# Kernel tuning notes

Hardware: AMD Instinct MI355X
Metric: run time of the kernel (lower is better)

The kernel has to match this reference:

```python
import jax, jax.numpy as jnp
import numpy as np

NUM_EXPERTS = 7
TRUNK_DIM = 64
HIDDEN = 64   # max(48, trunk_dim)
NUM_DEPTH_CLASSES = 3
BATCH = 262144


def setup_inputs() -> dict:
    key = jax.random.key(0)
    ks = jax.random.split(key, 8)
    trunk_feat = jax.random.normal(ks[0], (BATCH, TRUNK_DIM), dtype=jnp.float32)
    size_idx = jax.random.randint(ks[1], (BATCH,), 0, NUM_EXPERTS, dtype=jnp.int64)
    # Stacked expert MLP params: Linear(64,64) -> ReLU -> Linear(64,64) -> ReLU -> Linear(64,3)
    s1 = 1.0 / np.sqrt(TRUNK_DIM)
    s2 = 1.0 / np.sqrt(HIDDEN)
    W1 = jax.random.uniform(ks[2], (NUM_EXPERTS, TRUNK_DIM, HIDDEN), jnp.float32, -s1, s1)
    b1 = jax.random.uniform(ks[3], (NUM_EXPERTS, HIDDEN), jnp.float32, -s1, s1)
    W2 = jax.random.uniform(ks[4], (NUM_EXPERTS, HIDDEN, HIDDEN), jnp.float32, -s2, s2)
    b2 = jax.random.uniform(ks[5], (NUM_EXPERTS, HIDDEN), jnp.float32, -s2, s2)
    W3 = jax.random.uniform(ks[6], (NUM_EXPERTS, HIDDEN, NUM_DEPTH_CLASSES), jnp.float32, -s2, s2)
    b3 = jax.random.uniform(ks[7], (NUM_EXPERTS, NUM_DEPTH_CLASSES), jnp.float32, -s2, s2)
    return {"trunk_feat": trunk_feat, "size_idx": size_idx,
            "W1": W1, "b1": b1, "W2": W2, "b2": b2, "W3": W3, "b3": b3}


def _expert_mlp(x, W1, b1, W2, b2, W3, b3):
    # 3-layer MLP of one expert (dropout = identity in eval mode)
    h = jax.nn.relu(x @ W1 + b1)
    h = jax.nn.relu(h @ W2 + b2)
    return h @ W3 + b3  # [B, num_depth_classes]


def reference(trunk_feat, size_idx, W1, b1, W2, b2, W3, b3):
    # Hard routing (route_logits): rows with size_idx == e go through expert e;
    # expressed as masked accumulate so it is jit-friendly (no data-dependent shapes).
    B = trunk_feat.shape[0]
    logits = jnp.zeros((B, NUM_DEPTH_CLASSES), dtype=trunk_feat.dtype)
    for e in range(NUM_EXPERTS):  # fixed, small expert count
        le = _expert_mlp(trunk_feat, W1[e], b1[e], W2[e], b2[e], W3[e], b3[e])
        mask = (size_idx == e)[:, None]
        logits = logits + jnp.where(mask, le, jnp.zeros_like(le))
    probs = jax.nn.softmax(logits, axis=1)
    return logits, probs
```

## Files before the change

### kernel.cpp

```cpp
#include <hip/hip_runtime.h>
#include <stdint.h>

#define NE    7
#define DD    64
#define NDC   3
#define BLOCK 256
#define ROWS  256
#define NFRAG 18

typedef __fp16   half8 __attribute__((ext_vector_type(8)));
typedef float    f32x4 __attribute__((ext_vector_type(4)));
typedef uint32_t u32x4 __attribute__((ext_vector_type(4)));
typedef uint32_t u32x2 __attribute__((ext_vector_type(2)));
typedef __fp16   h2_t  __attribute__((ext_vector_type(2)));

__device__ __forceinline__ uint32_t pkrtz(float a, float b) {
  h2_t h = __builtin_amdgcn_cvt_pkrtz(a, b);
  return __builtin_bit_cast(uint32_t, h);
}
__device__ __forceinline__ f32x4 mfma16(u32x4 a, u32x4 b, f32x4 c) {
  return __builtin_amdgcn_mfma_f32_16x16x32_f16(
      __builtin_bit_cast(half8, a), __builtin_bit_cast(half8, b), c, 0, 0, 0);
}
__device__ __forceinline__ u32x4 relu_pack(f32x4 lo, f32x4 hi) {
  u32x4 t = { pkrtz(fmaxf(lo[0],0.f), fmaxf(lo[1],0.f)),
              pkrtz(fmaxf(lo[2],0.f), fmaxf(lo[3],0.f)),
              pkrtz(fmaxf(hi[0],0.f), fmaxf(hi[1],0.f)),
              pkrtz(fmaxf(hi[2],0.f), fmaxf(hi[3],0.f)) };
  return t;
}

__global__ __launch_bounds__(256) void pack_w2(
    const float* __restrict__ W1, const float* __restrict__ W2,
    const float* __restrict__ W3, uint32_t* __restrict__ ws) {
  __shared__ float wt[DD*DD];
  const int blk = blockIdx.x;
  const int e = blk >> 1, half = blk & 1;
  const float* Wsrc = (half ? W2 : W1) + (size_t)e*DD*DD;
  const float4* s4 = (const float4*)Wsrc;
  float4* d4 = (float4*)wt;
  #pragma unroll
  for (int i = 0; i < DD*DD/4/256; ++i)
    d4[i*256 + threadIdx.x] = s4[i*256 + threadIdx.x];
  __syncthreads();

  for (int idx = threadIdx.x; idx < 8*64; idx += 256) {
    const int fl = idx >> 6, l = idx & 63;
    const int nt = fl >> 1, ks = fl & 1;
    const int n  = nt*16 + (l & 15), g = l >> 4;
    uint32_t dst[4];
    #pragma unroll
    for (int d = 0; d < 4; ++d) {
      float v[2];
      #pragma unroll
      for (int h = 0; h < 2; ++h) {
        const int kk = 16*(d>>1) + 4*g + 2*(d&1) + h;
        v[h] = wt[(32*ks + kk)*DD + n];
      }
      dst[d] = pkrtz(v[0], v[1]);
    }
    uint32_t* p = ws + ((size_t)(e*NFRAG + half*8 + fl)*64 + l)*4;
    p[0]=dst[0]; p[1]=dst[1]; p[2]=dst[2]; p[3]=dst[3];
  }
  if (half == 0) {
    const float* Wl2 = W3 + (size_t)e*DD*NDC;
    for (int idx = threadIdx.x; idx < 2*64; idx += 256) {
      const int ks = idx >> 6, l = idx & 63;
      const int n  = l & 15, g = l >> 4;
      uint32_t dst[4];
      #pragma unroll
      for (int d = 0; d < 4; ++d) {
        float v[2];
        #pragma unroll
        for (int h = 0; h < 2; ++h) {
          const int kk = 16*(d>>1) + 4*g + 2*(d&1) + h;
          v[h] = (n < NDC) ? Wl2[(32*ks + kk)*NDC + n] : 0.0f;
        }
        dst[d] = pkrtz(v[0], v[1]);
      }
      uint32_t* p = ws + ((size_t)(e*NFRAG + 16 + ks)*64 + l)*4;
      p[0]=dst[0]; p[1]=dst[1]; p[2]=dst[2]; p[3]=dst[3];
    }
  }
}

__global__ __launch_bounds__(BLOCK, 3) void fused(
    const float* __restrict__ X, const int* __restrict__ S,
    const u32x4* __restrict__ wf,
    const float* __restrict__ b1, const float* __restrict__ b2,
    const float* __restrict__ b3,
    float* __restrict__ out, int B)
{
  __shared__ uint32_t pk[ROWS*32];
  __shared__ float    outbuf[ROWS*6];
  __shared__ uint16_t srt[ROWS];
  __shared__ int wcnt[4][NE], woff[4][NE], cnt[NE];

  const int tid  = threadIdx.x;
  const int wv   = tid >> 6, lane = tid & 63;
  const int r15  = lane & 15, g = lane >> 4;
  const int base = blockIdx.x * ROWS;

  u32x4 af[NFRAG];
  {
    const u32x4* wse = wf + (size_t)wv*NFRAG*64;
    #pragma unroll
    for (int f = 0; f < NFRAG; ++f) af[f] = wse[f*64 + lane];
  }

  const int e_i = S[base + tid];
  int myprefix = 0;
  {
    unsigned long long mk[NE];
    #pragma unroll
    for (int q2 = 0; q2 < NE; ++q2) mk[q2] = __ballot(e_i == q2);
    #pragma unroll
    for (int q2 = 0; q2 < NE; ++q2)
      if (e_i == q2) myprefix = __popcll(mk[q2] & ((1ull << lane) - 1ull));
    if (lane < NE) wcnt[wv][lane] = __popcll(mk[lane]);
  }

  {
    const float4* Xb = (const float4*)(X + (size_t)base * DD);
    #pragma unroll
    for (int it = 0; it < 16; ++it) {
      const int i = it*BLOCK + tid;
      const int r = i >> 4, q = i & 15;
      const float4 v = Xb[i];
      const int slotq = 4*(q >> 3) + (q & 3);
      const int hq    = (q >> 2) & 1;
      u32x2 w2 = { pkrtz(v.x, v.y), pkrtz(v.z, v.w) };
      *(u32x2*)&pk[r*32 + ((slotq ^ (r & 7)) << 2) + hq*2] = w2;
    }
  }
  __syncthreads();

  if (tid == 0) {
    int acc = 0;
    for (int q2 = 0; q2 < NE; ++q2) {
      const int s0 = acc;
      for (int w = 0; w < 4; ++w) { woff[w][q2] = acc; acc += wcnt[w][q2]; }
      cnt[q2] = acc - s0;
    }
  }
  __syncthreads();

  srt[woff[wv][e_i] + myprefix] = (uint16_t)tid;
  __syncthreads();

  auto run_expert = [&](int e, const u32x4 (&A)[NFRAG]) {
    const int cn    = cnt[e];
    const int sbase = woff[0][e];
    const float4 bv1[4] = { *(const float4*)(b1 + e*DD +  0 + 4*g),
                            *(const float4*)(b1 + e*DD + 16 + 4*g),
                            *(const float4*)(b1 + e*DD + 32 + 4*g),
                            *(const float4*)(b1 + e*DD + 48 + 4*g) };
    const float4 bv2[4] = { *(const float4*)(b2 + e*DD +  0 + 4*g),
                            *(const float4*)(b2 + e*DD + 16 + 4*g),
                            *(const float4*)(b2 + e*DD + 32 + 4*g),
                            *(const float4*)(b2 + e*DD + 48 + 4*g) };
    const float bb0 = b3[e*NDC+0], bb1 = b3[e*NDC+1], bb2 = b3[e*NDC+2];

    for (int r0 = 0; r0 < cn; r0 += 16) {
      const int m  = cn - r0;
      const int lr = srt[sbase + r0 + min(r15, m - 1)];

      const u32x4 xf0 = *(const u32x4*)&pk[lr*32 + (((    g) ^ (lr & 7)) << 2)];
      const u32x4 xf1 = *(const u32x4*)&pk[lr*32 + (((4 + g) ^ (lr & 7)) << 2)];

      f32x4 c[4];
      #pragma unroll
      for (int nt = 0; nt < 4; ++nt) {
        f32x4 acc = { bv1[nt].x, bv1[nt].y, bv1[nt].z, bv1[nt].w };
        acc = mfma16(A[nt*2 + 0], xf0, acc);
        acc = mfma16(A[nt*2 + 1], xf1, acc);
        c[nt] = acc;
      }
      const u32x4 h0 = relu_pack(c[0], c[1]);
      const u32x4 h1 = relu_pack(c[2], c[3]);

      #pragma unroll
      for (int nt = 0; nt < 4; ++nt) {
        f32x4 acc = { bv2[nt].x, bv2[nt].y, bv2[nt].z, bv2[nt].w };
        acc = mfma16(A[8 + nt*2 + 0], h0, acc);
        acc = mfma16(A[8 + nt*2 + 1], h1, acc);
        c[nt] = acc;
      }
      const u32x4 t0 = relu_pack(c[0], c[1]);
      const u32x4 t1 = relu_pack(c[2], c[3]);

      f32x4 acc = { bb0, bb1, bb2, 0.f };
      acc = mfma16(A[16], t0, acc);
      acc = mfma16(A[17], t1, acc);

      if (g == 0 && r15 < m) {
        const float l0 = acc[0], l1 = acc[1], l2 = acc[2];
        const float mx  = fmaxf(l0, fmaxf(l1, l2));
        const float p0  = __expf(l0 - mx);
        const float p1  = __expf(l1 - mx);
        const float p2  = __expf(l2 - mx);
        const float inv = 1.0f / (p0 + p1 + p2);
        float* ob = outbuf + lr*6;
        ob[0] = l0;     ob[1] = l1;     ob[2] = l2;
        ob[3] = p0*inv; ob[4] = p1*inv; ob[5] = p2*inv;
      }
    }
  };

  run_expert(wv, af);

  if (wv < 3) {
    const int e2 = wv + 4;
    const u32x4* wse2 = wf + (size_t)e2*NFRAG*64;
    #pragma unroll
    for (int f = 0; f < NFRAG; ++f) af[f] = wse2[f*64 + lane];
    run_expert(e2, af);
  }
  __syncthreads();

  #pragma unroll
  for (int it = 0; it < 3; ++it) {
    const int i = it*BLOCK + tid;
    const int r = i/3, c2 = i - r*3;
    out[(size_t)base*3 + i]               = outbuf[r*6 + c2];
    out[(size_t)B*3 + (size_t)base*3 + i] = outbuf[r*6 + 3 + c2];
  }
}

extern "C" void kernel_launch(void* const* d_in, const int* in_sizes, int n_in,
                              void* d_out, int out_size, void* d_ws, size_t ws_size,
                              hipStream_t stream)
{
  const float* X  = (const float*)d_in[0];
  const int*   S  = (const int*)d_in[1];
  const float* W1 = (const float*)d_in[2];
  const float* B1 = (const float*)d_in[3];
  const float* W2 = (const float*)d_in[4];
  const float* B2 = (const float*)d_in[5];
  const float* W3 = (const float*)d_in[6];
  const float* B3 = (const float*)d_in[7];
  float* out = (float*)d_out;
  uint32_t* ws = (uint32_t*)d_ws;

  const int B = in_sizes[0] / DD;

  pack_w2<<<NE*2, 256, 0, stream>>>(W1, W2, W3, ws);
  fused<<<B / ROWS, BLOCK, 0, stream>>>(X, S, (const u32x4*)ws,
                                        B1, B2, B3, out, B);
}
```

Before: 34.86 us.

## Write outputs directly to global, parallelize expert offset scan, reorder routing prologue

```diff
diff --git a/kernel.cpp b/kernel.cpp
--- a/kernel.cpp
+++ b/kernel.cpp
@@ -92,7 +92,6 @@
     float* __restrict__ out, int B)
 {
   __shared__ uint32_t pk[ROWS*32];
-  __shared__ float    outbuf[ROWS*6];
   __shared__ uint16_t srt[ROWS];
   __shared__ int wcnt[4][NE], woff[4][NE], cnt[NE];
 
@@ -101,23 +100,13 @@
   const int r15  = lane & 15, g = lane >> 4;
   const int base = blockIdx.x * ROWS;
 
+  const int e_i = S[base + tid];
+
   u32x4 af[NFRAG];
   {
     const u32x4* wse = wf + (size_t)wv*NFRAG*64;
     #pragma unroll
     for (int f = 0; f < NFRAG; ++f) af[f] = wse[f*64 + lane];
-  }
-
-  const int e_i = S[base + tid];
-  int myprefix = 0;
-  {
-    unsigned long long mk[NE];
-    #pragma unroll
-    for (int q2 = 0; q2 < NE; ++q2) mk[q2] = __ballot(e_i == q2);
-    #pragma unroll
-    for (int q2 = 0; q2 < NE; ++q2)
-      if (e_i == q2) myprefix = __popcll(mk[q2] & ((1ull << lane) - 1ull));
-    if (lane < NE) wcnt[wv][lane] = __popcll(mk[lane]);
   }
 
   {
@@ -133,15 +122,33 @@
       *(u32x2*)&pk[r*32 + ((slotq ^ (r & 7)) << 2) + hq*2] = w2;
     }
   }
-  __syncthreads();
-
-  if (tid == 0) {
-    int acc = 0;
-    for (int q2 = 0; q2 < NE; ++q2) {
-      const int s0 = acc;
-      for (int w = 0; w < 4; ++w) { woff[w][q2] = acc; acc += wcnt[w][q2]; }
-      cnt[q2] = acc - s0;
-    }
+
+  int myprefix = 0;
+  {
+    unsigned long long mk[NE];
+    #pragma unroll
+    for (int q2 = 0; q2 < NE; ++q2) mk[q2] = __ballot(e_i == q2);
+    #pragma unroll
+    for (int q2 = 0; q2 < NE; ++q2)
+      if (e_i == q2) myprefix = __popcll(mk[q2] & ((1ull << lane) - 1ull));
+    if (lane < NE) wcnt[wv][lane] = __popcll(mk[lane]);
+  }
+  __syncthreads();
+
+  if (wv == 0) {
+    const int i = lane;
+    int v = (i < 4*NE) ? wcnt[i & 3][i >> 2] : 0;
+    int incl = v;
+    #pragma unroll
+    for (int d2 = 1; d2 < 32; d2 <<= 1) {
+      const int t2 = __shfl_up(incl, d2, 64);
+      if (lane >= d2) incl += t2;
+    }
+    const int excl = incl - v;
+    if (i < 4*NE) woff[i & 3][i >> 2] = excl;
+    const int incl3 = __shfl(incl, 4*lane + 3, 64);
+    const int excl0 = __shfl(excl, 4*lane,     64);
+    if (i < NE) cnt[i] = incl3 - excl0;
   }
   __syncthreads();
 
@@ -194,15 +201,17 @@
       acc = mfma16(A[17], t1, acc);
 
       if (g == 0 && r15 < m) {
+        const int row = base + lr;
         const float l0 = acc[0], l1 = acc[1], l2 = acc[2];
         const float mx  = fmaxf(l0, fmaxf(l1, l2));
         const float p0  = __expf(l0 - mx);
         const float p1  = __expf(l1 - mx);
         const float p2  = __expf(l2 - mx);
         const float inv = 1.0f / (p0 + p1 + p2);
-        float* ob = outbuf + lr*6;
-        ob[0] = l0;     ob[1] = l1;     ob[2] = l2;
-        ob[3] = p0*inv; ob[4] = p1*inv; ob[5] = p2*inv;
+        float* o = out + (size_t)row*3;
+        o[0] = l0; o[1] = l1; o[2] = l2;
+        float* pr = out + (size_t)B*3 + (size_t)row*3;
+        pr[0] = p0*inv; pr[1] = p1*inv; pr[2] = p2*inv;
       }
     }
   };
@@ -215,15 +224,6 @@
     #pragma unroll
     for (int f = 0; f < NFRAG; ++f) af[f] = wse2[f*64 + lane];
     run_expert(e2, af);
-  }
-  __syncthreads();
-
-  #pragma unroll
-  for (int it = 0; it < 3; ++it) {
-    const int i = it*BLOCK + tid;
-    const int r = i/3, c2 = i - r*3;
-    out[(size_t)base*3 + i]               = outbuf[r*6 + c2];
-    out[(size_t)B*3 + (size_t)base*3 + i] = outbuf[r*6 + 3 + c2];
   }
 }
 
```

Measured after the change: 29.65 us, median of 2. -14.9%, faster.
